# Optimization experiments

Measured on AMD Instinct MI355X. Metric: run time of the kernel, lower is better.

## Reference

```python
import jax, jax.numpy as jnp
import numpy as np

D_MODEL = 2048
NUM_HEADS = 16
NUM_KV_HEADS = 4
HEAD_DIM = D_MODEL // NUM_HEADS
ROPE_THETA = 10000.0


def setup_inputs() -> dict:
    key = jax.random.key(0)
    ks = jax.random.split(key, 5)
    B, S = 2, 2048
    scale = 0.02
    return {
        "x": jax.random.normal(ks[0], (B, S, D_MODEL), dtype=jnp.float32),
        "wq": jax.random.normal(ks[1], (D_MODEL, NUM_HEADS * HEAD_DIM), dtype=jnp.float32) * scale,
        "wk": jax.random.normal(ks[2], (D_MODEL, NUM_KV_HEADS * HEAD_DIM), dtype=jnp.float32) * scale,
        "wv": jax.random.normal(ks[3], (D_MODEL, NUM_KV_HEADS * HEAD_DIM), dtype=jnp.float32) * scale,
        "wo": jax.random.normal(ks[4], (NUM_HEADS * HEAD_DIM, D_MODEL), dtype=jnp.float32) * scale,
    }


def _rope_cos_sin(seq_len, head_dim, dtype):
    # Llama-style: freqs over even indices, angles = pos * inv_freq
    inv_freq = 1.0 / (ROPE_THETA ** (jnp.arange(0, head_dim, 2, dtype=jnp.float32) / head_dim))
    ang = jnp.arange(seq_len, dtype=jnp.float32)[:, None] * inv_freq[None, :]  # [S, hd/2]
    cos = jnp.cos(ang).astype(dtype)[None, :, None, :]  # [1,S,1,hd/2]
    sin = jnp.sin(ang).astype(dtype)[None, :, None, :]
    return cos, sin


def _apply_rope(x, cos, sin):
    # x: [B,S,H,hd]; interleaved complex rotation on pairs (x[2i], x[2i+1])
    x1 = x[..., 0::2]
    x2 = x[..., 1::2]
    y1 = x1 * cos - x2 * sin
    y2 = x1 * sin + x2 * cos
    return jnp.stack([y1, y2], axis=-1).reshape(x.shape)


def reference(x, wq, wk, wv, wo):
    B, S, D = x.shape
    H, KV, hd = NUM_HEADS, NUM_KV_HEADS, HEAD_DIM
    g = H // KV
    q = (x @ wq).reshape(B, S, H, hd)
    k = (x @ wk).reshape(B, S, KV, hd)
    v = (x @ wv).reshape(B, S, KV, hd)
    cos, sin = _rope_cos_sin(S, hd, x.dtype)
    q = _apply_rope(q, cos, sin)
    k = _apply_rope(k, cos, sin)
    q = q.transpose(0, 2, 1, 3)  # [B,H,S,hd]
    k = k.transpose(0, 2, 1, 3)  # [B,KV,S,hd]
    v = v.transpose(0, 2, 1, 3)
    k = jnp.repeat(k, g, axis=1)  # GQA: [B,H,S,hd]
    v = jnp.repeat(v, g, axis=1)
    attn = jnp.einsum('bqsh,bqlh->bqsl', q, k) * (1.0 / np.sqrt(hd)).astype(np.float32)
    attn = jax.nn.softmax(attn, axis=-1)  # non-causal, as in source
    out = jnp.einsum('bqsl,bqlh->bqsh', attn, v)
    out = out.transpose(0, 2, 1, 3).reshape(B, S, D)
    return out @ wo
```

## Files before the change

### kernel.cpp

```cpp
#include <hip/hip_runtime.h>


typedef __attribute__((ext_vector_type(8))) short short8;
typedef __attribute__((ext_vector_type(4))) float f32x4;

#define DEV static __device__ __forceinline__

#define NB 2
#define NS 2048
#define ND 2048
#define NH 16
#define NKV 4
#define HD 128
#define NQKV 3072

DEV unsigned short f2bf(float f) {
  union { float f; unsigned u; } v; v.f = f;
  unsigned r = v.u + 0x7fffu + ((v.u >> 16) & 1u);
  return (unsigned short)(r >> 16);
}
DEV unsigned short f2bf_fast(float f) {
  union { float f; unsigned u; } v; v.f = f;
  return (unsigned short)((v.u + 0x8000u) >> 16);
}
DEV float bf2f(unsigned short u) {
  union { unsigned u; float f; } v; v.u = ((unsigned)u) << 16; return v.f;
}
DEV unsigned pack2bf(float a, float b) {
  return (unsigned)f2bf_fast(a) | ((unsigned)f2bf_fast(b) << 16);
}
DEV unsigned pack2bf_rne(float a, float b) {
  return (unsigned)f2bf(a) | ((unsigned)f2bf(b) << 16);
}

DEV void swap32(unsigned &x, unsigned &y) {
  asm volatile("v_permlane32_swap_b32 %0, %1" : "+v"(x), "+v"(y));
}
DEV void swap16(unsigned &x, unsigned &y) {
  asm volatile("v_permlane16_swap_b32 %0, %1" : "+v"(x), "+v"(y));
}

typedef const __attribute__((address_space(1))) void* gas1_t;
typedef __attribute__((address_space(3))) void* las3_t;
DEV void gload16(const void* g, void* l) {
  __builtin_amdgcn_global_load_lds((gas1_t)g, (las3_t)l, 16, 0, 0);
}

DEV f32x4 mfma16(short8 a, short8 b, f32x4 c) {
  return __builtin_amdgcn_mfma_f32_16x16x32_bf16(a, b, c, 0, 0, 0);
}


__global__ __launch_bounds__(256) void convert_x_kernel(const float* __restrict__ x,
                                                        unsigned short* __restrict__ xb) {
  size_t i = ((size_t)blockIdx.x * 256 + threadIdx.x) * 4;
  float4 v = *(const float4*)(x + i);
  unsigned long long pack = (unsigned long long)f2bf(v.x)
                          | ((unsigned long long)f2bf(v.y) << 16)
                          | ((unsigned long long)f2bf(v.z) << 32)
                          | ((unsigned long long)f2bf(v.w) << 48);
  *(unsigned long long*)(xb + i) = pack;
}

__global__ __launch_bounds__(256) void transpose_w_kernel(const float* __restrict__ src,
                                                          unsigned short* __restrict__ dst,
                                                          int K, int N) {
  __shared__ float tile[64][65];
  const int k0 = blockIdx.x * 64, n0 = blockIdx.y * 64;
  for (int i = threadIdx.x; i < 4096; i += 256) {
    int r = i >> 6, c = i & 63;
    tile[r][c] = src[(size_t)(k0 + r) * N + n0 + c];
  }
  __syncthreads();
  for (int i = threadIdx.x; i < 4096; i += 256) {
    int r = i >> 6, c = i & 63;
    dst[(size_t)(n0 + r) * K + k0 + c] = f2bf(tile[c][r]);
  }
}

__global__ __launch_bounds__(256) void rope_table_kernel(float2* __restrict__ tab) {
  int t = blockIdx.x * 256 + threadIdx.x;
  int s = t >> 6, i = t & 63;
  float freq = powf(10000.0f, -(float)i * (1.0f / 64.0f));
  float ang = (float)s * freq;
  tab[t] = make_float2(cosf(ang), sinf(ang));
}

__global__ __launch_bounds__(256) void rope_scatter_kernel(const unsigned short* __restrict__ QKV,
                                                           const float2* __restrict__ tab,
                                                           unsigned short* __restrict__ Qb,
                                                           unsigned short* __restrict__ Kb) {
  int t = blockIdx.x * 256 + threadIdx.x;
  const float qscale = 0.12751741161895452f;
  if (t < (1 << 22)) {
    int i = t & 63, h = (t >> 6) & 15, s = (t >> 10) & 2047, b = t >> 21;
    const unsigned short* p = QKV + (size_t)(b * NS + s) * NQKV + h * HD + 2 * i;
    float2 cs = tab[s * 64 + i];
    float x1 = bf2f(p[0]), x2 = bf2f(p[1]);
    unsigned short* q = Qb + (size_t)((b * NH + h) * NS + s) * HD + 2 * i;
    q[0] = f2bf((x1 * cs.x - x2 * cs.y) * qscale);
    q[1] = f2bf((x1 * cs.y + x2 * cs.x) * qscale);
  } else {
    int u = t - (1 << 22);
    int i = u & 63, kv = (u >> 6) & 3, s = (u >> 8) & 2047, b = u >> 19;
    const unsigned short* p = QKV + (size_t)(b * NS + s) * NQKV + 2048 + kv * HD + 2 * i;
    float2 cs = tab[s * 64 + i];
    float x1 = bf2f(p[0]), x2 = bf2f(p[1]);
    unsigned short* k = Kb + (size_t)((b * NKV + kv) * NS + s) * HD + 2 * i;
    k[0] = f2bf(x1 * cs.x - x2 * cs.y);
    k[1] = f2bf(x1 * cs.y + x2 * cs.x);
  }
}

__global__ __launch_bounds__(256) void transpose_v_kernel(const unsigned short* __restrict__ QKV,
                                                          unsigned short* __restrict__ Vt) {
  __shared__ unsigned short tile[64][65];
  const int bk = blockIdx.x, b = bk >> 2, kv = bk & 3;
  const int s0 = blockIdx.y * 64, d0 = blockIdx.z * 64;
  for (int i = threadIdx.x; i < 4096; i += 256) {
    int r = i >> 6, c = i & 63;
    tile[r][c] = QKV[(size_t)(b * NS + s0 + r) * NQKV + 2560 + kv * HD + d0 + c];
  }
  __syncthreads();
  for (int i = threadIdx.x; i < 4096; i += 256) {
    int r = i >> 6, c = i & 63;
    Vt[(size_t)((b * NKV + kv) * HD + d0 + r) * NS + s0 + c] = tile[c][r];
  }
}


template <int N, bool OUTBF16>
__global__ __launch_bounds__(256) void gemm_kernel(const unsigned short* __restrict__ A,
                                                   const unsigned short* __restrict__ Bt,
                                                   void* __restrict__ Cout) {
  __shared__ unsigned short As[128 * 32];
  __shared__ unsigned short Bs[128 * 32];
  const int K = 2048;
  const int tid = threadIdx.x, wid = tid >> 6, lane = tid & 63;
  const int wm = wid >> 1, wn = wid & 1;
  const int m0 = blockIdx.x * 128, n0 = blockIdx.y * 128;
  f32x4 acc[4][4] = {};
  const int srow = tid >> 2;
  const int scol = (tid & 3) * 8;
  const unsigned short* Ab = A + (size_t)(m0 + srow) * K + scol;
  const unsigned short* Ab2 = Ab + (size_t)64 * K;
  const unsigned short* Bb = Bt + (size_t)(n0 + srow) * K + scol;
  const unsigned short* Bb2 = Bb + (size_t)64 * K;

  for (int kt = 0; kt < K; kt += 32) {
    gload16(Ab + kt, &As[wid * 512]);
    gload16(Ab2 + kt, &As[2048 + wid * 512]);
    gload16(Bb + kt, &Bs[wid * 512]);
    gload16(Bb2 + kt, &Bs[2048 + wid * 512]);
    __syncthreads();
    short8 af[4], bfr[4];
#pragma unroll
    for (int r = 0; r < 4; ++r)
      af[r] = *(const short8*)&As[(wm * 64 + r * 16 + (lane & 15)) * 32 + (lane >> 4) * 8];
#pragma unroll
    for (int c = 0; c < 4; ++c)
      bfr[c] = *(const short8*)&Bs[(wn * 64 + c * 16 + (lane & 15)) * 32 + (lane >> 4) * 8];
    __builtin_amdgcn_s_setprio(1);
#pragma unroll
    for (int r = 0; r < 4; ++r)
#pragma unroll
      for (int c = 0; c < 4; ++c)
        acc[r][c] = mfma16(af[r], bfr[c], acc[r][c]);
    __builtin_amdgcn_s_setprio(0);
    __syncthreads();
  }

  if (OUTBF16) {
    unsigned short* C = (unsigned short*)Cout;
#pragma unroll
    for (int r = 0; r < 4; ++r) {
      const int row = m0 + wm * 64 + r * 16 + (lane >> 4) * 4;
#pragma unroll
      for (int c = 0; c < 4; ++c) {
        const int col = n0 + wn * 64 + c * 16 + (lane & 15);
#pragma unroll
        for (int j = 0; j < 4; ++j)
          C[(size_t)(row + j) * N + col] = f2bf(acc[r][c][j]);
      }
    }
  } else {
    float* C = (float*)Cout;
#pragma unroll
    for (int r = 0; r < 4; ++r) {
      const int row = m0 + wm * 64 + r * 16 + (lane >> 4) * 4;
#pragma unroll
      for (int c = 0; c < 4; ++c) {
        const int col = n0 + wn * 64 + c * 16 + (lane & 15);
#pragma unroll
        for (int j = 0; j < 4; ++j)
          C[(size_t)(row + j) * N + col] = acc[r][c][j];
      }
    }
  }
}


__global__ __launch_bounds__(256, 2) void attn_kernel(const unsigned short* __restrict__ Qb,
                                                      const unsigned short* __restrict__ Kb,
                                                      const unsigned short* __restrict__ Vt,
                                                      unsigned short* __restrict__ O) {
  __shared__ unsigned short Ks[2][64 * 128];
  __shared__ unsigned short Vs[2][128 * 64];
  const int tid = threadIdx.x, wid = tid >> 6, lane = tid & 63;
  const int blk = blockIdx.x;
  const int qt = blk & 15, h = (blk >> 4) & 15, b = blk >> 8;
  const int kvh = h >> 2;
  const int q0 = qt * 128 + wid * 32;

  const unsigned short* qhead = Qb + (size_t)((b * NH + h) * NS) * HD;
  const unsigned short* khead = Kb + (size_t)((b * NKV + kvh) * NS) * HD;
  const unsigned short* vhead = Vt + (size_t)((b * NKV + kvh) * HD) * NS;

  const int cl = lane & 15, g4 = (lane >> 4) * 4, hi8 = (lane >> 4) * 8;
  const int swk = (lane & 7) << 3;

  auto stageKV = [&](int buf, int kt) {
#pragma unroll
    for (int i = 0; i < 4; ++i) {
      int row = i * 16 + (tid >> 4);
      int col = ((tid & 15) * 8) ^ ((row & 7) << 3);
      gload16(khead + (size_t)(kt + row) * HD + col, &Ks[buf][i * 2048 + wid * 512]);
    }
#pragma unroll
    for (int i = 0; i < 4; ++i) {
      int row = i * 32 + (tid >> 3);
      int col = ((tid & 7) * 8) ^ ((row & 7) << 3);
      gload16(vhead + (size_t)row * NS + kt + col, &Vs[buf][i * 2048 + wid * 512]);
    }
  };

  stageKV(0, 0);

  short8 qf[2][4];
#pragma unroll
  for (int r = 0; r < 2; ++r)
#pragma unroll
    for (int kk = 0; kk < 4; ++kk)
      qf[r][kk] = *(const short8*)(qhead + (size_t)(q0 + r * 16 + cl) * HD + kk * 32 + hi8);

  f32x4 od[2][8] = {};
  float mrun[2] = {-1e30f, -1e30f}, lpart[2] = {0.f, 0.f};

  int cur = 0;
  for (int it = 0; it < NS / 64; ++it) {
    if (it + 1 < NS / 64) {
      stageKV(cur ^ 1, (it + 1) * 64);
      asm volatile("s_waitcnt vmcnt(8)" ::: "memory");
    } else {
      asm volatile("s_waitcnt vmcnt(0)" ::: "memory");
    }
    __builtin_amdgcn_s_barrier();

    const unsigned short* ks = Ks[cur];
    const unsigned short* vs = Vs[cur];

    f32x4 s[2][4];
#pragma unroll
    for (int r = 0; r < 2; ++r)
#pragma unroll
      for (int c4 = 0; c4 < 4; ++c4) s[r][c4] = f32x4{0.f, 0.f, 0.f, 0.f};
    __builtin_amdgcn_s_setprio(1);
#pragma unroll
    for (int c4 = 0; c4 < 4; ++c4)
#pragma unroll
      for (int kk = 0; kk < 4; ++kk) {
        short8 kf = *(const short8*)&ks[((c4 * 16 + cl) * 128 + kk * 32 + hi8) ^ swk];
        s[0][c4] = mfma16(kf, qf[0][kk], s[0][c4]);
        s[1][c4] = mfma16(kf, qf[1][kk], s[1][c4]);
      }
    __builtin_amdgcn_s_setprio(0);

    float mt[2];
#pragma unroll
    for (int r = 0; r < 2; ++r) {
      float m = fmaxf(fmaxf(fmaxf(s[r][0][0], s[r][0][1]), fmaxf(s[r][0][2], s[r][0][3])),
                      fmaxf(fmaxf(s[r][1][0], s[r][1][1]), fmaxf(s[r][1][2], s[r][1][3])));
      float m2 = fmaxf(fmaxf(fmaxf(s[r][2][0], s[r][2][1]), fmaxf(s[r][2][2], s[r][2][3])),
                       fmaxf(fmaxf(s[r][3][0], s[r][3][1]), fmaxf(s[r][3][2], s[r][3][3])));
      m = fmaxf(m, m2);
      m = fmaxf(m, __shfl_xor(m, 16, 64));
      m = fmaxf(m, __shfl_xor(m, 32, 64));
      mt[r] = m;
    }
    bool need = (mt[0] > mrun[0] + 8.0f) || (mt[1] > mrun[1] + 8.0f);
    if (__any(need)) {
#pragma unroll
      for (int r = 0; r < 2; ++r) {
        float mn = fmaxf(mrun[r], mt[r]);
        float corr = __builtin_amdgcn_exp2f(mrun[r] - mn);
        mrun[r] = mn;
        lpart[r] *= corr;
#pragma unroll
        for (int c = 0; c < 8; ++c)
          od[r][c] *= corr;
      }
    }
#pragma unroll
    for (int r = 0; r < 2; ++r) {
      float acc = 0.f;
#pragma unroll
      for (int c4 = 0; c4 < 4; ++c4)
#pragma unroll
        for (int j = 0; j < 4; ++j) {
          float p = __builtin_amdgcn_exp2f(s[r][c4][j] - mrun[r]);
          s[r][c4][j] = p;
          acc += p;
        }
      lpart[r] += acc;
    }

    short8 pb[2][2];
#pragma unroll
    for (int r = 0; r < 2; ++r) {
      unsigned w00 = pack2bf(s[r][0][0], s[r][0][1]), w01 = pack2bf(s[r][0][2], s[r][0][3]);
      unsigned w10 = pack2bf(s[r][1][0], s[r][1][1]), w11 = pack2bf(s[r][1][2], s[r][1][3]);
      unsigned w20 = pack2bf(s[r][2][0], s[r][2][1]), w21 = pack2bf(s[r][2][2], s[r][2][3]);
      unsigned w30 = pack2bf(s[r][3][0], s[r][3][1]), w31 = pack2bf(s[r][3][2], s[r][3][3]);
      union { unsigned u[4]; short8 v; } t0, t1;
      swap32(w00, w10); swap16(w00, w10); t0.u[0] = w00; t0.u[2] = w10;
      swap32(w01, w11); swap16(w01, w11); t0.u[1] = w01; t0.u[3] = w11;
      swap32(w20, w30); swap16(w20, w30); t1.u[0] = w20; t1.u[2] = w30;
      swap32(w21, w31); swap16(w21, w31); t1.u[1] = w21; t1.u[3] = w31;
      pb[r][0] = t0.v;
      pb[r][1] = t1.v;
    }

    __builtin_amdgcn_s_setprio(1);
#pragma unroll
    for (int c = 0; c < 8; ++c) {
      const int rr = c * 16 + cl;
      short8 vf0 = *(const short8*)&vs[(rr * 64 + hi8) ^ swk];
      short8 vf1 = *(const short8*)&vs[(rr * 64 + 32 + hi8) ^ swk];
      od[0][c] = mfma16(vf0, pb[0][0], od[0][c]);
      od[0][c] = mfma16(vf1, pb[0][1], od[0][c]);
      od[1][c] = mfma16(vf0, pb[1][0], od[1][c]);
      od[1][c] = mfma16(vf1, pb[1][1], od[1][c]);
    }
    __builtin_amdgcn_s_setprio(0);
    __builtin_amdgcn_s_barrier();
    cur ^= 1;
  }

  float linv[2];
#pragma unroll
  for (int r = 0; r < 2; ++r) {
    float l = lpart[r];
    l += __shfl_xor(l, 16, 64);
    l += __shfl_xor(l, 32, 64);
    linv[r] = 1.0f / l;
  }
#pragma unroll
  for (int r = 0; r < 2; ++r) {
    const size_t row = (size_t)(b * NS + q0 + 16 * r + cl);
#pragma unroll
    for (int c = 0; c < 8; ++c) {
      uint2 pk;
      pk.x = pack2bf_rne(od[r][c][0] * linv[r], od[r][c][1] * linv[r]);
      pk.y = pack2bf_rne(od[r][c][2] * linv[r], od[r][c][3] * linv[r]);
      *(uint2*)(O + row * ND + h * HD + c * 16 + g4) = pk;
    }
  }
}


extern "C" void kernel_launch(void* const* d_in, const int* in_sizes, int n_in,
                              void* d_out, int out_size, void* d_ws, size_t ws_size,
                              hipStream_t stream) {
  const float* x  = (const float*)d_in[0];
  const float* wq = (const float*)d_in[1];
  const float* wk = (const float*)d_in[2];
  const float* wv = (const float*)d_in[3];
  const float* wo = (const float*)d_in[4];
  float* out = (float*)d_out;
  char* ws = (char*)d_ws;

  unsigned short* xb   = (unsigned short*)(ws + 0);
  unsigned short* wT   = (unsigned short*)(ws + 16777216);
  unsigned short* woT  = (unsigned short*)(ws + 29360128);
  float2*         tab  = (float2*)(ws + 37748736);
  unsigned short* QKV  = (unsigned short*)(ws + 38797312);
  unsigned short* Qb   = xb;
  unsigned short* Kb   = wT;
  unsigned short* Vt   = (unsigned short*)(ws + 16777216 + 4194304);
  unsigned short* Obuf = QKV;

  convert_x_kernel<<<8192, 256, 0, stream>>>(x, xb);
  transpose_w_kernel<<<dim3(32, 32), 256, 0, stream>>>(wq, wT, 2048, 2048);
  transpose_w_kernel<<<dim3(32, 8),  256, 0, stream>>>(wk, wT + (size_t)2048 * 2048, 2048, 512);
  transpose_w_kernel<<<dim3(32, 8),  256, 0, stream>>>(wv, wT + (size_t)2560 * 2048, 2048, 512);
  transpose_w_kernel<<<dim3(32, 32), 256, 0, stream>>>(wo, woT, 2048, 2048);
  rope_table_kernel<<<512, 256, 0, stream>>>(tab);

  gemm_kernel<NQKV, true><<<dim3(32, 24), 256, 0, stream>>>(xb, wT, QKV);

  rope_scatter_kernel<<<20480, 256, 0, stream>>>(QKV, tab, Qb, Kb);
  transpose_v_kernel<<<dim3(8, 32, 2), 256, 0, stream>>>(QKV, Vt);

  attn_kernel<<<512, 256, 0, stream>>>(Qb, Kb, Vt, Obuf);

  gemm_kernel<ND, false><<<dim3(32, 16), 256, 0, stream>>>(Obuf, woT, out);
}
```

Measured before the change: 248.4 us.

## Deepen GEMM K-tile with XOR-swizzled LDS, grid swizzle, and hardware bf16 pack

The GEMM kernel now stages 64-wide K tiles instead of 32, which halves the number of barrier pairs per K loop. LDS reads and writes use an XOR swizzle to avoid bank conflicts, and the block index is remapped so neighbouring workgroups share A/B tiles in L2. Separately, the attention kernel's software bf16 packing is replaced by the v_cvt_pk_bf16_f32 instruction, which changes rounding from round-half-up to the hardware mode. The larger LDS footprint per block may reduce occupancy.

```diff
diff --git a/kernel.cpp b/kernel.cpp
--- a/kernel.cpp
+++ b/kernel.cpp
@@ -19,18 +19,16 @@
   unsigned r = v.u + 0x7fffu + ((v.u >> 16) & 1u);
   return (unsigned short)(r >> 16);
 }
-DEV unsigned short f2bf_fast(float f) {
-  union { float f; unsigned u; } v; v.f = f;
-  return (unsigned short)((v.u + 0x8000u) >> 16);
-}
 DEV float bf2f(unsigned short u) {
   union { unsigned u; float f; } v; v.u = ((unsigned)u) << 16; return v.f;
 }
-DEV unsigned pack2bf(float a, float b) {
-  return (unsigned)f2bf_fast(a) | ((unsigned)f2bf_fast(b) << 16);
-}
 DEV unsigned pack2bf_rne(float a, float b) {
   return (unsigned)f2bf(a) | ((unsigned)f2bf(b) << 16);
+}
+DEV unsigned cvtpk(float a, float b) {
+  unsigned r;
+  asm("v_cvt_pk_bf16_f32 %0, %1, %2" : "=v"(r) : "v"(a), "v"(b));
+  return r;
 }
 
 DEV void swap32(unsigned &x, unsigned &y) {
@@ -133,39 +131,54 @@
 __global__ __launch_bounds__(256) void gemm_kernel(const unsigned short* __restrict__ A,
                                                    const unsigned short* __restrict__ Bt,
                                                    void* __restrict__ Cout) {
-  __shared__ unsigned short As[128 * 32];
-  __shared__ unsigned short Bs[128 * 32];
+  __shared__ unsigned short As[128 * 64];
+  __shared__ unsigned short Bs[128 * 64];
   const int K = 2048;
   const int tid = threadIdx.x, wid = tid >> 6, lane = tid & 63;
   const int wm = wid >> 1, wn = wid & 1;
-  const int m0 = blockIdx.x * 128, n0 = blockIdx.y * 128;
+
+  const int nwg = gridDim.x * gridDim.y;
+  const int bid = blockIdx.y * gridDim.x + blockIdx.x;
+  const int swzb = (bid & 7) * (nwg >> 3) + (bid >> 3);
+  const int m0 = (swzb % gridDim.x) * 128;
+  const int n0 = (swzb / gridDim.x) * 128;
+
   f32x4 acc[4][4] = {};
-  const int srow = tid >> 2;
-  const int scol = (tid & 3) * 8;
-  const unsigned short* Ab = A + (size_t)(m0 + srow) * K + scol;
-  const unsigned short* Ab2 = Ab + (size_t)64 * K;
-  const unsigned short* Bb = Bt + (size_t)(n0 + srow) * K + scol;
-  const unsigned short* Bb2 = Bb + (size_t)64 * K;
-
-  for (int kt = 0; kt < K; kt += 32) {
-    gload16(Ab + kt, &As[wid * 512]);
-    gload16(Ab2 + kt, &As[2048 + wid * 512]);
-    gload16(Bb + kt, &Bs[wid * 512]);
-    gload16(Bb2 + kt, &Bs[2048 + wid * 512]);
+  const int cl = lane & 15, hi8 = (lane >> 4) * 8;
+  const int swg = (cl & 7) << 3;
+
+  const int srow = lane >> 3;
+  const int scol = ((lane & 7) * 8) ^ (srow << 3);
+  const unsigned short* PA = A + (size_t)(m0 + wid * 8 + srow) * K + scol;
+  const unsigned short* PB = Bt + (size_t)(n0 + wid * 8 + srow) * K + scol;
+
+  for (int kt = 0; kt < K; kt += 64) {
+#pragma unroll
+    for (int i = 0; i < 4; ++i)
+      gload16(PA + (size_t)(i * 32) * K + kt, &As[i * 2048 + wid * 512]);
+#pragma unroll
+    for (int i = 0; i < 4; ++i)
+      gload16(PB + (size_t)(i * 32) * K + kt, &Bs[i * 2048 + wid * 512]);
     __syncthreads();
-    short8 af[4], bfr[4];
-#pragma unroll
-    for (int r = 0; r < 4; ++r)
-      af[r] = *(const short8*)&As[(wm * 64 + r * 16 + (lane & 15)) * 32 + (lane >> 4) * 8];
-#pragma unroll
-    for (int c = 0; c < 4; ++c)
-      bfr[c] = *(const short8*)&Bs[(wn * 64 + c * 16 + (lane & 15)) * 32 + (lane >> 4) * 8];
+
+    short8 af[2][4], bfr[2][4];
+#pragma unroll
+    for (int kk = 0; kk < 2; ++kk) {
+#pragma unroll
+      for (int r = 0; r < 4; ++r)
+        af[kk][r] = *(const short8*)&As[(wm * 64 + r * 16 + cl) * 64 + ((kk * 32 + hi8) ^ swg)];
+#pragma unroll
+      for (int c = 0; c < 4; ++c)
+        bfr[kk][c] = *(const short8*)&Bs[(wn * 64 + c * 16 + cl) * 64 + ((kk * 32 + hi8) ^ swg)];
+    }
     __builtin_amdgcn_s_setprio(1);
 #pragma unroll
-    for (int r = 0; r < 4; ++r)
-#pragma unroll
-      for (int c = 0; c < 4; ++c)
-        acc[r][c] = mfma16(af[r], bfr[c], acc[r][c]);
+    for (int kk = 0; kk < 2; ++kk)
+#pragma unroll
+      for (int r = 0; r < 4; ++r)
+#pragma unroll
+        for (int c = 0; c < 4; ++c)
+          acc[r][c] = mfma16(af[kk][r], bfr[kk][c], acc[r][c]);
     __builtin_amdgcn_s_setprio(0);
     __syncthreads();
   }
@@ -177,7 +190,7 @@
       const int row = m0 + wm * 64 + r * 16 + (lane >> 4) * 4;
 #pragma unroll
       for (int c = 0; c < 4; ++c) {
-        const int col = n0 + wn * 64 + c * 16 + (lane & 15);
+        const int col = n0 + wn * 64 + c * 16 + cl;
 #pragma unroll
         for (int j = 0; j < 4; ++j)
           C[(size_t)(row + j) * N + col] = f2bf(acc[r][c][j]);
@@ -190,7 +203,7 @@
       const int row = m0 + wm * 64 + r * 16 + (lane >> 4) * 4;
 #pragma unroll
       for (int c = 0; c < 4; ++c) {
-        const int col = n0 + wn * 64 + c * 16 + (lane & 15);
+        const int col = n0 + wn * 64 + c * 16 + cl;
 #pragma unroll
         for (int j = 0; j < 4; ++j)
           C[(size_t)(row + j) * N + col] = acc[r][c][j];
@@ -317,10 +330,10 @@
     short8 pb[2][2];
 #pragma unroll
     for (int r = 0; r < 2; ++r) {
-      unsigned w00 = pack2bf(s[r][0][0], s[r][0][1]), w01 = pack2bf(s[r][0][2], s[r][0][3]);
-      unsigned w10 = pack2bf(s[r][1][0], s[r][1][1]), w11 = pack2bf(s[r][1][2], s[r][1][3]);
-      unsigned w20 = pack2bf(s[r][2][0], s[r][2][1]), w21 = pack2bf(s[r][2][2], s[r][2][3]);
-      unsigned w30 = pack2bf(s[r][3][0], s[r][3][1]), w31 = pack2bf(s[r][3][2], s[r][3][3]);
+      unsigned w00 = cvtpk(s[r][0][0], s[r][0][1]), w01 = cvtpk(s[r][0][2], s[r][0][3]);
+      unsigned w10 = cvtpk(s[r][1][0], s[r][1][1]), w11 = cvtpk(s[r][1][2], s[r][1][3]);
+      unsigned w20 = cvtpk(s[r][2][0], s[r][2][1]), w21 = cvtpk(s[r][2][2], s[r][2][3]);
+      unsigned w30 = cvtpk(s[r][3][0], s[r][3][1]), w31 = cvtpk(s[r][3][2], s[r][3][3]);
       union { unsigned u[4]; short8 v; } t0, t1;
       swap32(w00, w10); swap16(w00, w10); t0.u[0] = w00; t0.u[2] = w10;
       swap32(w01, w11); swap16(w01, w11); t0.u[1] = w01; t0.u[3] = w11;
```

Result: faster. 240.8 us (-3.1%).
